# Kernel tuning notes

Measured on AMD Instinct MI355X. Metric: run time of the kernel, lower is better.

The kernel has to match this reference:

```python
import jax, jax.numpy as jnp
import numpy as np

# Dimensions (match init_kwargs / input_specs)
B, T, H, S, R, E = 4, 2048, 1024, 512, 16, 4
F = 6 + 2 * R           # engine_state_feature_dim
ETA = 0.1               # impression_rate
ACC_DECAY = 0.99        # accumulator EMA decay
EPS = 1e-6


def setup_inputs() -> dict:
    key = jax.random.key(0)
    ks = jax.random.split(key, 20)
    n = jax.random.normal
    x = n(ks[0], (B, T, H), jnp.float32)
    # ComplexLinear signal_proj: hidden -> state
    sig_Wr = n(ks[1], (H, S), jnp.float32) / np.sqrt(H).astype(np.float32)
    sig_Wi = n(ks[2], (H, S), jnp.float32) / np.sqrt(H).astype(np.float32)
    sig_br = jnp.zeros((S,), jnp.float32)
    sig_bi = jnp.zeros((S,), jnp.float32)
    # Per-engine complex state projection [E, S, R] and diagonal complex decay [E, R]
    A_r = n(ks[3], (E, S, R), jnp.float32) / np.sqrt(S).astype(np.float32)
    A_i = n(ks[4], (E, S, R), jnp.float32) / np.sqrt(S).astype(np.float32)
    mag = 0.90 + 0.09 * jax.random.uniform(ks[5], (E, R), jnp.float32)
    ph = (2.0 * np.pi) * jax.random.uniform(ks[6], (E, R), jnp.float32)
    lam_r = mag * jnp.cos(ph)
    lam_i = mag * jnp.sin(ph)
    # Per-engine ComplexLinear: feature(F) -> hidden(H)
    eh_Wr = n(ks[7], (E, F, H), jnp.float32) / np.sqrt(F).astype(np.float32)
    eh_Wi = n(ks[8], (E, F, H), jnp.float32) / np.sqrt(F).astype(np.float32)
    eh_br = jnp.zeros((E, H), jnp.float32)
    eh_bi = jnp.zeros((E, H), jnp.float32)
    # Engine fusion ComplexLinear: E*H -> H
    fu_Wr = n(ks[9], (E * H, H), jnp.float32) / np.sqrt(E * H).astype(np.float32)
    fu_Wi = n(ks[10], (E * H, H), jnp.float32) / np.sqrt(E * H).astype(np.float32)
    fu_br = jnp.zeros((H,), jnp.float32)
    fu_bi = jnp.zeros((H,), jnp.float32)
    # Gate: Linear(4H -> H)
    g_W = n(ks[11], (4 * H, H), jnp.float32) / np.sqrt(4 * H).astype(np.float32)
    g_b = jnp.zeros((H,), jnp.float32)
    return dict(x=x, sig_Wr=sig_Wr, sig_Wi=sig_Wi, sig_br=sig_br, sig_bi=sig_bi,
                A_r=A_r, A_i=A_i, lam_r=lam_r, lam_i=lam_i,
                eh_Wr=eh_Wr, eh_Wi=eh_Wi, eh_br=eh_br, eh_bi=eh_bi,
                fu_Wr=fu_Wr, fu_Wi=fu_Wi, fu_br=fu_br, fu_bi=fu_bi,
                g_W=g_W, g_b=g_b)


def _run_engines(ur, ui, lam_r, lam_i):
    """Complex diagonal recurrence over time for all engines jointly.
    ur, ui: [E,B,T,R] complex drive. Returns per-step features [E,B,T,F] (real, imag)."""
    lr = lam_r[:, None, :]  # [E,1,R]
    li = lam_i[:, None, :]

    def step(carry, u):
        hr, hi, acc = carry                      # [E,B,R], [E,B,R], [E,B]
        ur_t, ui_t = u                           # [E,B,R]
        nhr = (1.0 - ETA) * (lr * hr - li * hi) + ETA * ur_t
        nhi = (1.0 - ETA) * (lr * hi + li * hr) + ETA * ui_t
        mag2 = nhr * nhr + nhi * nhi             # [E,B,R]
        m_mean = jnp.mean(mag2, axis=-1)         # [E,B]
        nacc = ACC_DECAY * acc + (1.0 - ACC_DECAY) * m_mean
        inv = jax.lax.rsqrt(m_mean + EPS)[..., None]
        hnr, hni = nhr * inv, nhi * inv          # rms-normalized complex state
        z = jnp.zeros_like(m_mean)
        scal_r = jnp.stack([hnr.mean(-1), hni.mean(-1),
                            jnp.sqrt(m_mean + EPS),
                            jnp.sqrt(jnp.max(mag2, axis=-1) + EPS),
                            nacc, jnp.log1p(nacc)], axis=-1)   # [E,B,6]
        scal_i = jnp.stack([hni.mean(-1), -hnr.mean(-1), z, z, z, z], axis=-1)
        fr = jnp.concatenate([scal_r, hnr, hni], axis=-1)      # [E,B,F]
        fi = jnp.concatenate([scal_i, hni, -hnr], axis=-1)
        return (nhr, nhi, nacc), (fr, fi)

    init = (jnp.zeros((E, B, R), ur.dtype), jnp.zeros((E, B, R), ur.dtype),
            jnp.zeros((E, B), ur.dtype))
    u_seq = (jnp.moveaxis(ur, 2, 0), jnp.moveaxis(ui, 2, 0))   # [T,E,B,R]
    _, (frs, fis) = jax.lax.scan(step, init, u_seq)
    return jnp.moveaxis(frs, 0, 2), jnp.moveaxis(fis, 0, 2)    # [E,B,T,F]


def reference(x, sig_Wr, sig_Wi, sig_br, sig_bi, A_r, A_i, lam_r, lam_i,
              eh_Wr, eh_Wi, eh_br, eh_bi, fu_Wr, fu_Wi, fu_br, fu_bi, g_W, g_b):
    # Complex signal projection of real input: z = (Wr + i Wi)^T x + b
    zr = x @ sig_Wr + sig_br                     # [B,T,S]
    zi = x @ sig_Wi + sig_bi
    # Complex per-engine drive u = A^H-style complex matmul: [E,B,T,R]
    ur = jnp.einsum('bts,esr->ebtr', zr, A_r) - jnp.einsum('bts,esr->ebtr', zi, A_i)
    ui = jnp.einsum('bts,esr->ebtr', zr, A_i) + jnp.einsum('bts,esr->ebtr', zi, A_r)
    fr, fi = _run_engines(ur, ui, lam_r, lam_i)  # [E,B,T,F]
    # Per-engine ComplexLinear feature -> hidden
    yr = (jnp.einsum('ebtf,efh->ebth', fr, eh_Wr)
          - jnp.einsum('ebtf,efh->ebth', fi, eh_Wi)) + eh_br[:, None, None, :]
    yi = (jnp.einsum('ebtf,efh->ebth', fr, eh_Wi)
          + jnp.einsum('ebtf,efh->ebth', fi, eh_Wr)) + eh_bi[:, None, None, :]
    # Concat engines along feature axis -> [B,T,E*H]
    yr_c = jnp.moveaxis(yr, 0, 2).reshape(B, T, E * H)
    yi_c = jnp.moveaxis(yi, 0, 2).reshape(B, T, E * H)
    # Engine fusion ComplexLinear
    frf = yr_c @ fu_Wr - yi_c @ fu_Wi + fu_br    # [B,T,H]
    fif = yr_c @ fu_Wi + yi_c @ fu_Wr + fu_bi
    mag = jnp.sqrt(frf * frf + fif * fif + EPS)
    g = jax.nn.sigmoid(jnp.concatenate([x, frf, fif, mag], axis=-1) @ g_W + g_b)
    return g * frf + (1.0 - g) * x
```

## Files before the change

kernel.cpp:

```cpp
#include <hip/hip_runtime.h>
#include <stdint.h>

#define B_ 4
#define T_ 2048
#define H_ 1024
#define S_ 512
#define R_ 16
#define E_ 4
#define F_ 38
#define BT_ (B_*T_)
#define KF_ 320

typedef __attribute__((ext_vector_type(8))) __bf16 bf16x8;
typedef __attribute__((ext_vector_type(4))) float f32x4;

static __device__ __forceinline__ unsigned short f2bf(float f) {
    unsigned int u = __float_as_uint(f);
    unsigned int r = (u + 0x7fffu + ((u >> 16) & 1u)) >> 16;
    return (unsigned short)r;
}

static __device__ __forceinline__ void gload_lds16(const unsigned short* g, unsigned short* l) {
    __builtin_amdgcn_global_load_lds(
        (const __attribute__((address_space(1))) unsigned int*)g,
        (__attribute__((address_space(3))) unsigned int*)l, 16, 0, 0);
}

template<int EPI, int DEPTH>
__global__ __launch_bounds__(256) void k_gemm(
    const unsigned short* __restrict__ A, int lda,
    const unsigned short* __restrict__ BT, int ldb,
    float* __restrict__ C, int ldc,
    const float* __restrict__ bias, int K,
    size_t sA, size_t sB, size_t sC, size_t sA2, size_t sB2, int nbx,
    const float* __restrict__ aux1, const float* __restrict__ aux2,
    unsigned short* __restrict__ auxO)
{
    const int z1 = blockIdx.z >> 2, z0 = blockIdx.z & 3;
    A  += (size_t)z1 * sA + (size_t)z0 * sA2;
    BT += (size_t)z1 * sB + (size_t)z0 * sB2;
    C  += (size_t)z1 * sC;

    int bx, by;
    {
        const int f = blockIdx.x;
        const int nwg = gridDim.x;
        int s;
        if ((nwg & 7) == 0) {
            const int q = nwg >> 3;
            s = (f & 7) * q + (f >> 3);
        } else s = f;
        by = s / nbx; bx = s - by * nbx;
    }

    __shared__ unsigned short As[DEPTH * 4096];
    __shared__ unsigned short Bs[DEPTH * 4096];
    const int tid = threadIdx.x;
    const int l = tid & 63;
    const int wv = tid >> 6;
    const int wm = wv >> 1, wn = wv & 1;
    const int m16 = l & 15, kg = l >> 4;
    const size_t bm = (size_t)by * 128;
    const size_t bn = (size_t)bx * 128;

    const int slab0 = wv * 2, slab1 = wv * 2 + 1;
    const int rIn = l >> 2;
    const int kOff = (l & 3) * 8;
    const unsigned short* gA0 = A + (bm + slab0 * 16 + rIn) * (size_t)lda + kOff;
    const unsigned short* gA1 = A + (bm + slab1 * 16 + rIn) * (size_t)lda + kOff;
    const unsigned short* gB0 = BT + (bn + slab0 * 16 + rIn) * (size_t)ldb + kOff;
    const unsigned short* gB1 = BT + (bn + slab1 * 16 + rIn) * (size_t)ldb + kOff;
    const int sOffA0 = slab0 * 512, sOffA1 = slab1 * 512;

    f32x4 acc[4][4];
#pragma unroll
    for (int i = 0; i < 4; ++i)
#pragma unroll
        for (int j = 0; j < 4; ++j) acc[i][j] = (f32x4){0.f, 0.f, 0.f, 0.f};

    const int nkt = K >> 5;
#pragma unroll
    for (int p = 0; p < DEPTH - 1; ++p) {
        if (p < nkt) {
            const int o = p * 4096;
            gload_lds16(gA0, As + o + sOffA0);
            gload_lds16(gA1, As + o + sOffA1);
            gload_lds16(gB0, Bs + o + sOffA0);
            gload_lds16(gB1, Bs + o + sOffA1);
            gA0 += 32; gA1 += 32; gB0 += 32; gB1 += 32;
        }
    }

    for (int kt = 0; kt < nkt; ++kt) {
        __builtin_amdgcn_s_barrier();
        if (kt + DEPTH - 1 < nkt) {
            const int o = ((kt + DEPTH - 1) % DEPTH) * 4096;
            gload_lds16(gA0, As + o + sOffA0);
            gload_lds16(gA1, As + o + sOffA1);
            gload_lds16(gB0, Bs + o + sOffA0);
            gload_lds16(gB1, Bs + o + sOffA1);
            gA0 += 32; gA1 += 32; gB0 += 32; gB1 += 32;
        }
        const int rem = nkt - 1 - kt;
        const int ahead = rem < (DEPTH - 1) ? rem : (DEPTH - 1);
        if (ahead >= 3)      asm volatile("s_waitcnt vmcnt(12)" ::: "memory");
        else if (ahead == 2) asm volatile("s_waitcnt vmcnt(8)" ::: "memory");
        else if (ahead == 1) asm volatile("s_waitcnt vmcnt(4)" ::: "memory");
        else                 asm volatile("s_waitcnt vmcnt(0)" ::: "memory");
        __builtin_amdgcn_s_barrier();

        const int cur = (kt % DEPTH) * 4096;
        bf16x8 af[4], bfr[4];
#pragma unroll
        for (int i = 0; i < 4; ++i)
            af[i] = *(const bf16x8*)&As[cur + (wm * 64 + i * 16 + m16) * 32 + kg * 8];
#pragma unroll
        for (int j = 0; j < 4; ++j)
            bfr[j] = *(const bf16x8*)&Bs[cur + (wn * 64 + j * 16 + m16) * 32 + kg * 8];
#pragma unroll
        for (int i = 0; i < 4; ++i)
#pragma unroll
            for (int j = 0; j < 4; ++j)
                acc[i][j] = __builtin_amdgcn_mfma_f32_16x16x32_bf16(af[i], bfr[j], acc[i][j], 0, 0, 0);
    }

#pragma unroll
    for (int j = 0; j < 4; ++j) {
        const size_t col = bn + wn * 64 + j * 16 + m16;
        const float bv = (EPI == 1 || EPI == 4) ? 0.f : (bias ? bias[col] : 0.f);
#pragma unroll
        for (int i = 0; i < 4; ++i) {
            const size_t row0 = bm + wm * 64 + i * 16 + kg * 4;
#pragma unroll
            for (int p = 0; p < 4; ++p) {
                const size_t row = row0 + p;
                if constexpr (EPI == 0) {
                    C[row * (size_t)ldc + col] = acc[i][j][p] + bv;
                } else if constexpr (EPI == 1) {
                    atomicAdd(&C[row * (size_t)ldc + col], acc[i][j][p]);
                } else if constexpr (EPI == 4) {
                    atomicAdd(&C[col * (size_t)ldc + row], acc[i][j][p]);
                } else if constexpr (EPI == 2) {
                    const float v = acc[i][j][p] + bv;
                    const float w = __shfl_xor(v, 1, 64);
                    const int h = (int)(col >> 1);
                    if ((col & 1) == 0) {
                        C[row * 1024 + h] = v;
                        auxO[row * 4096 + 1024 + h] = f2bf(v);
                    } else {
                        auxO[row * 4096 + 2048 + h] = f2bf(v);
                        auxO[row * 4096 + 3072 + h] = f2bf(sqrtf(w * w + v * v + 1e-6f));
                    }
                } else {
                    const float z = acc[i][j][p] + bv;
                    const float g = 1.f / (1.f + __expf(-z));
                    const float fr = aux1[row * 1024 + col];
                    const float xv = aux2[row * 1024 + col];
                    C[row * 1024 + col] = fmaf(g, fr - xv, xv);
                }
            }
        }
    }
}

__global__ __launch_bounds__(256) void k_cast_x(const float* __restrict__ x,
                                                unsigned short* __restrict__ Abig)
{
    const int gid = blockIdx.x * 256 + threadIdx.x;
    const int row = gid >> 8;
    const int c4 = (gid & 255) << 2;
    float4 v = *(const float4*)&x[(size_t)row * H_ + c4];
    ushort4 o;
    o.x = f2bf(v.x); o.y = f2bf(v.y); o.z = f2bf(v.z); o.w = f2bf(v.w);
    *(ushort4*)&Abig[(size_t)row * 4096 + c4] = o;
}

__global__ __launch_bounds__(256) void k_gwt(const float* __restrict__ gW,
                                             unsigned short* __restrict__ gWT)
{
    __shared__ float tile[32][33];
    const int tx = threadIdx.x & 31, ty = threadIdx.x >> 5;
    const int k0 = blockIdx.x * 32, n0 = blockIdx.y * 32;
#pragma unroll
    for (int q = 0; q < 4; ++q) {
        int kk = ty * 4 + q;
        tile[kk][tx] = gW[(size_t)(k0 + kk) * H_ + n0 + tx];
    }
    __syncthreads();
#pragma unroll
    for (int q = 0; q < 4; ++q) {
        int nn = ty * 4 + q;
        gWT[(size_t)(n0 + nn) * 4096 + k0 + tx] = f2bf(tile[tx][nn]);
    }
}

__global__ __launch_bounds__(64) void k_wu(const float* __restrict__ sigWr,
                                           const float* __restrict__ sigWi,
                                           const float* __restrict__ A_r,
                                           const float* __restrict__ A_i,
                                           unsigned short* __restrict__ WuT)
{
    __shared__ float swr[S_], swi[S_];
    const int h = blockIdx.x;
    const int tid = threadIdx.x;
    for (int s = tid; s < S_; s += 64) {
        swr[s] = sigWr[(size_t)h * S_ + s];
        swi[s] = sigWi[(size_t)h * S_ + s];
    }
    __syncthreads();
    const int e = tid >> 4, r = tid & 15;
    float a0 = 0.f, a1 = 0.f;
    for (int s = 0; s < S_; ++s) {
        float ar = A_r[((size_t)(e * S_ + s)) * R_ + r];
        float ai = A_i[((size_t)(e * S_ + s)) * R_ + r];
        float wr = swr[s], wi = swi[s];
        a0 += wr * ar - wi * ai;
        a1 += wr * ai + wi * ar;
    }
    WuT[(size_t)tid * H_ + h] = f2bf(a0);
    WuT[(size_t)(64 + tid) * H_ + h] = f2bf(a1);
}

__global__ __launch_bounds__(64) void k_bu(const float* __restrict__ sigbr,
                                           const float* __restrict__ sigbi,
                                           const float* __restrict__ A_r,
                                           const float* __restrict__ A_i,
                                           float* __restrict__ b_u)
{
    const int n = blockIdx.x;
    const int lane = threadIdx.x;
    const int m = n & 63;
    const int e = m >> 4, r = m & 15;
    const bool hi = n >= 64;
    float acc = 0.f;
    for (int s = lane; s < S_; s += 64) {
        float ar = A_r[((size_t)(e * S_ + s)) * R_ + r];
        float ai = A_i[((size_t)(e * S_ + s)) * R_ + r];
        float br = sigbr[s], bi = sigbi[s];
        acc += hi ? (br * ai + bi * ar) : (br * ar - bi * ai);
    }
#pragma unroll
    for (int st = 32; st; st >>= 1) acc += __shfl_down(acc, st, 64);
    if (lane == 0) b_u[n] = acc;
}

__global__ __launch_bounds__(256) void k_uinit(const float* __restrict__ b_u,
                                               float* __restrict__ U)
{
    const int gid = blockIdx.x * 256 + threadIdx.x;
    U[gid] = b_u[gid >> 13];
}

__global__ __launch_bounds__(256) void k_prepA(const float* __restrict__ ehWr,
                                               const float* __restrict__ ehWi,
                                               const float* __restrict__ ehbr,
                                               const float* __restrict__ ehbi,
                                               unsigned short* __restrict__ Ac)
{
    const int gid = blockIdx.x * 256 + threadIdx.x;
    const int e = gid >> 16;
    const int rem = gid & 65535;
    const int row = rem >> 9;
    const int k = (rem & 511) << 2;
    float4 f = {0.f, 0.f, 0.f, 0.f};
    if (row < F_) {
        const float* src = (k < 1024) ? ehWr + ((size_t)(e * F_ + row)) * 1024 + k
                                      : ehWi + ((size_t)(e * F_ + row)) * 1024 + (k - 1024);
        f = *(const float4*)src;
    } else if (row == F_) {
        const float* src = (k < 1024) ? ehbr + (size_t)e * 1024 + k
                                      : ehbi + (size_t)e * 1024 + (k - 1024);
        f = *(const float4*)src;
    }
    ushort4 o;
    o.x = f2bf(f.x); o.y = f2bf(f.y); o.z = f2bf(f.z); o.w = f2bf(f.w);
    *(ushort4*)&Ac[(size_t)gid * 4] = o;
}

__global__ __launch_bounds__(256) void k_prepB(const float* __restrict__ fuWr,
                                               const float* __restrict__ fuWi,
                                               unsigned short* __restrict__ Bc)
{
    __shared__ float tR[32][33], tI[32][33];
    const int e = blockIdx.z;
    const int k0 = blockIdx.x * 32;
    const int h0 = blockIdx.y * 32;
    const int tx = threadIdx.x & 31, ty = threadIdx.x >> 5;
    const float* fr = fuWr + ((size_t)e * 1024 + k0) * 1024 + h0;
    const float* fi = fuWi + ((size_t)e * 1024 + k0) * 1024 + h0;
#pragma unroll
    for (int q = 0; q < 4; ++q) {
        int kk = ty * 4 + q;
        tR[kk][tx] = fr[(size_t)kk * 1024 + tx];
        tI[kk][tx] = fi[(size_t)kk * 1024 + tx];
    }
    __syncthreads();
    unsigned short* Be = Bc + (size_t)e * 2048 * 2048;
#pragma unroll
    for (int q = 0; q < 4; ++q) {
        int rr = ty * 4 + q;
        float vR = tR[tx][rr], vI = tI[tx][rr];
        size_t rowLo = (size_t)(h0 + rr) * 2048;
        size_t rowHi = (size_t)(1024 + h0 + rr) * 2048;
        Be[rowLo + k0 + tx]        = f2bf(vR);
        Be[rowLo + 1024 + k0 + tx] = f2bf(-vI);
        Be[rowHi + k0 + tx]        = f2bf(vI);
        Be[rowHi + 1024 + k0 + tx] = f2bf(vR);
    }
}

__global__ __launch_bounds__(256) void k_w2t(const float* __restrict__ C,
                                             unsigned short* __restrict__ W2T)
{
    const int gid = blockIdx.x * 256 + threadIdx.x;
    const int n = gid / KF_;
    const int k = gid - n * KF_;
    const int h = n >> 1;
    const int s = n & 1;
    float v = 0.f;
    if (k < 304) {
        const int fp = (k < 152) ? k : k - 152;
        const int e = fp / F_;
        const int f = fp - e * F_;
        const float* Ce = C + ((size_t)e * 128 + f) * 2048;
        const float mr = Ce[h], mi = Ce[1024 + h];
        if (s == 0) v = (k < 152) ? mr : -mi;
        else        v = (k < 152) ? mi :  mr;
    }
    W2T[gid] = f2bf(v);
}

__global__ __launch_bounds__(256) void k_b2(const float* __restrict__ fubr,
                                            const float* __restrict__ fubi,
                                            const float* __restrict__ C,
                                            float* __restrict__ b2)
{
    const int n = blockIdx.x * 256 + threadIdx.x;
    const int h = n >> 1;
    const int s = n & 1;
    const int colOld = s * 1024 + h;
    float v = s ? fubi[h] : fubr[h];
#pragma unroll
    for (int e = 0; e < 4; ++e)
        v += C[(size_t)e * 128 * 2048 + (size_t)F_ * 2048 + colOld];
    b2[n] = v;
}

__global__ __launch_bounds__(64) void k_scan(const float* __restrict__ U,
                                             const float* __restrict__ lam_r,
                                             const float* __restrict__ lam_i,
                                             float* __restrict__ Hr, float* __restrict__ Hi)
{
    const int wid = blockIdx.x;
    const int b = wid >> 6, ch = wid & 63;
    const int lane = threadIdx.x;
    const float cr = 0.9f * lam_r[ch];
    const float ci = 0.9f * lam_i[ch];
    const float* Ur = U + (size_t)ch * BT_ + (size_t)b * T_;
    const float* Uc = U + (size_t)(64 + ch) * BT_ + (size_t)b * T_;
    const int t0 = lane * 32;
    float ur[32], ui[32];
#pragma unroll
    for (int q = 0; q < 8; ++q) {
        float4 vr = *(const float4*)&Ur[t0 + q * 4];
        float4 vi = *(const float4*)&Uc[t0 + q * 4];
        ur[q*4+0]=vr.x; ur[q*4+1]=vr.y; ur[q*4+2]=vr.z; ur[q*4+3]=vr.w;
        ui[q*4+0]=vi.x; ui[q*4+1]=vi.y; ui[q*4+2]=vi.z; ui[q*4+3]=vi.w;
    }
    float hr = 0.f, hi = 0.f;
#pragma unroll
    for (int j = 0; j < 32; ++j) {
        float nr = fmaf(cr, hr, fmaf(-ci, hi, 0.1f * ur[j]));
        float ni = fmaf(cr, hi, fmaf(ci, hr, 0.1f * ui[j]));
        hr = nr; hi = ni;
    }
    float dr = cr, di = ci;
#pragma unroll
    for (int q = 0; q < 5; ++q) { float t = dr*dr - di*di; di = 2.f*dr*di; dr = t; }
    float xr = hr, xi = hi;
#pragma unroll
    for (int st = 1; st < 64; st <<= 1) {
        float yr = __shfl_up(xr, (unsigned)st, 64);
        float yi = __shfl_up(xi, (unsigned)st, 64);
        if (lane >= st) {
            float nxr = fmaf(dr, yr, fmaf(-di, yi, xr));
            float nxi = fmaf(dr, yi, fmaf(di, yr, xi));
            xr = nxr; xi = nxi;
        }
        float t = dr*dr - di*di; di = 2.f*dr*di; dr = t;
    }
    float ir = __shfl_up(xr, 1u, 64);
    float ii = __shfl_up(xi, 1u, 64);
    if (lane == 0) { ir = 0.f; ii = 0.f; }
    hr = ir; hi = ii;
    float* HrB = Hr + (size_t)b * T_ * 64;
    float* HiB = Hi + (size_t)b * T_ * 64;
#pragma unroll
    for (int j = 0; j < 32; ++j) {
        float nr = fmaf(cr, hr, fmaf(-ci, hi, 0.1f * ur[j]));
        float ni = fmaf(cr, hi, fmaf(ci, hr, 0.1f * ui[j]));
        HrB[(size_t)(t0 + j) * 64 + ch] = nr;
        HiB[(size_t)(t0 + j) * 64 + ch] = ni;
        hr = nr; hi = ni;
    }
}

__global__ __launch_bounds__(256) void k_feat(const float* __restrict__ Hr,
                                              const float* __restrict__ Hi,
                                              unsigned short* __restrict__ Fcat,
                                              float* __restrict__ Mbuf)
{
    const int gid = blockIdx.x * 256 + threadIdx.x;
    const int e = gid & 3;
    const int bt = gid >> 2;
    const float* hr = Hr + (size_t)bt * 64 + e * 16;
    const float* hi = Hi + (size_t)bt * 64 + e * 16;
    float nr[16], ni[16];
#pragma unroll
    for (int q = 0; q < 4; ++q) {
        float4 vr = ((const float4*)hr)[q];
        float4 vi = ((const float4*)hi)[q];
        nr[q*4+0]=vr.x; nr[q*4+1]=vr.y; nr[q*4+2]=vr.z; nr[q*4+3]=vr.w;
        ni[q*4+0]=vi.x; ni[q*4+1]=vi.y; ni[q*4+2]=vi.z; ni[q*4+3]=vi.w;
    }
    float sum = 0.f, mx = 0.f, sr = 0.f, si = 0.f;
#pragma unroll
    for (int i = 0; i < 16; ++i) {
        float m2 = nr[i] * nr[i] + ni[i] * ni[i];
        sum += m2; mx = fmaxf(mx, m2);
        sr += nr[i]; si += ni[i];
    }
    const float mm = sum * 0.0625f;
    const float inv = rsqrtf(mm + 1e-6f);
    const int b = bt >> 11, t = bt & (T_ - 1);
    Mbuf[(size_t)(e * 4 + b) * T_ + t] = mm;
    unsigned short* Fp = Fcat + (size_t)bt * KF_;
    const int br = e * F_, bi2 = 152 + e * F_;
    const float mhr = sr * 0.0625f * inv;
    const float mhi = si * 0.0625f * inv;
    Fp[br + 0] = f2bf(mhr);
    Fp[br + 1] = f2bf(mhi);
    Fp[br + 2] = f2bf(sqrtf(mm + 1e-6f));
    Fp[br + 3] = f2bf(sqrtf(mx + 1e-6f));
    Fp[bi2 + 0] = f2bf(mhi);
    Fp[bi2 + 1] = f2bf(-mhr);
#pragma unroll
    for (int i = 0; i < 16; ++i) {
        float a = nr[i] * inv, c = ni[i] * inv;
        Fp[br + 6 + i]   = f2bf(a);
        Fp[br + 22 + i]  = f2bf(c);
        Fp[bi2 + 6 + i]  = f2bf(c);
        Fp[bi2 + 22 + i] = f2bf(-a);
    }
}

__global__ __launch_bounds__(256) void k_acc(const float* __restrict__ Mbuf,
                                             unsigned short* __restrict__ Fcat)
{
    const int w = blockIdx.x * 4 + (threadIdx.x >> 6);
    const int lane = threadIdx.x & 63;
    const int e = w >> 2, b = w & 3;
    const float* mp = Mbuf + (size_t)(e * 4 + b) * T_ + lane * 32;
    float m[32];
#pragma unroll
    for (int j = 0; j < 32; ++j) m[j] = mp[j];
    float s = 0.f;
#pragma unroll
    for (int j = 0; j < 32; ++j) s = fmaf(0.99f, s, 0.01f * m[j]);
    float d = 0.99f;
#pragma unroll
    for (int q = 0; q < 5; ++q) d = d * d;
    float x = s;
#pragma unroll
    for (int st = 1; st < 64; st <<= 1) {
        float y = __shfl_up(x, (unsigned)st, 64);
        if (lane >= st) x = fmaf(d, y, x);
        d = d * d;
    }
    float init = __shfl_up(x, 1u, 64);
    if (lane == 0) init = 0.f;
    float acc = init;
#pragma unroll
    for (int j = 0; j < 32; ++j) {
        acc = fmaf(0.99f, acc, 0.01f * m[j]);
        const int t = lane * 32 + j;
        size_t ro = ((size_t)(b * T_ + t)) * KF_ + e * F_;
        Fcat[ro + 4] = f2bf(acc);
        Fcat[ro + 5] = f2bf(log1pf(acc));
    }
}

extern "C" void kernel_launch(void* const* d_in, const int* in_sizes, int n_in,
                              void* d_out, int out_size, void* d_ws, size_t ws_size,
                              hipStream_t stream)
{
    const float* x     = (const float*)d_in[0];
    const float* sigWr = (const float*)d_in[1];
    const float* sigWi = (const float*)d_in[2];
    const float* sigbr = (const float*)d_in[3];
    const float* sigbi = (const float*)d_in[4];
    const float* A_r   = (const float*)d_in[5];
    const float* A_i   = (const float*)d_in[6];
    const float* lam_r = (const float*)d_in[7];
    const float* lam_i = (const float*)d_in[8];
    const float* ehWr  = (const float*)d_in[9];
    const float* ehWi  = (const float*)d_in[10];
    const float* ehbr  = (const float*)d_in[11];
    const float* ehbi  = (const float*)d_in[12];
    const float* fuWr  = (const float*)d_in[13];
    const float* fuWi  = (const float*)d_in[14];
    const float* fubr  = (const float*)d_in[15];
    const float* fubi  = (const float*)d_in[16];
    const float* gW    = (const float*)d_in[17];
    const float* gb    = (const float*)d_in[18];

    char* ws = (char*)d_ws;
    size_t off = 0;
    auto alloc = [&](size_t bytes) -> void* {
        void* p = ws + off;
        off = (off + bytes + 255) & ~(size_t)255;
        return p;
    };
    unsigned short* Abig = (unsigned short*)alloc((size_t)BT_ * 4096 * 2);
    float* FRFr          = (float*)alloc((size_t)BT_ * 1024 * 4);
    unsigned short* Fcat = (unsigned short*)alloc((size_t)BT_ * KF_ * 2);
    float* U             = (float*)alloc((size_t)BT_ * 128 * 4);
    float* Hr            = (float*)alloc((size_t)BT_ * 64 * 4);
    float* Hi            = (float*)alloc((size_t)BT_ * 64 * 4);
    float* Mbuf          = (float*)alloc((size_t)16 * T_ * 4);
    unsigned short* WuT  = (unsigned short*)alloc((size_t)128 * H_ * 2);
    float* b_u           = (float*)alloc(128 * 4);
    unsigned short* W2T  = (unsigned short*)alloc((size_t)2048 * KF_ * 2);
    float* b2            = (float*)alloc(2048 * 4);
    unsigned short* gWT  = (unsigned short*)alloc((size_t)H_ * 4096 * 2);
    unsigned short* Acomp= (unsigned short*)alloc((size_t)4 * 128 * 2048 * 2);
    unsigned short* Bcomp= (unsigned short*)alloc((size_t)4 * 2048 * 2048 * 2);
    float* Ccomp         = (float*)alloc((size_t)4 * 128 * 2048 * 4);
    if (off > ws_size) return;

    hipMemsetAsync(Fcat, 0, (size_t)BT_ * KF_ * 2, stream);
    hipMemsetAsync(Ccomp, 0, (size_t)4 * 128 * 2048 * 4, stream);

    k_cast_x<<<dim3(BT_ * H_ / 4 / 256), dim3(256), 0, stream>>>(x, Abig);
    k_gwt<<<dim3(128, 32), dim3(256), 0, stream>>>(gW, gWT);
    k_wu<<<dim3(H_), dim3(64), 0, stream>>>(sigWr, sigWi, A_r, A_i, WuT);
    k_bu<<<dim3(128), dim3(64), 0, stream>>>(sigbr, sigbi, A_r, A_i, b_u);
    k_prepA<<<dim3(1024), dim3(256), 0, stream>>>(ehWr, ehWi, ehbr, ehbi, Acomp);
    k_prepB<<<dim3(32, 32, 4), dim3(256), 0, stream>>>(fuWr, fuWi, Bcomp);

    k_gemm<1, 4><<<dim3(16, 1, 16), dim3(256), 0, stream>>>(
        Acomp, 2048, Bcomp, 2048, Ccomp, 2048, (const float*)nullptr, 512,
        (size_t)128 * 2048, (size_t)2048 * 2048, (size_t)128 * 2048,
        (size_t)512, (size_t)512, 16, nullptr, nullptr, nullptr);

    k_w2t<<<dim3(2048 * KF_ / 256), dim3(256), 0, stream>>>(Ccomp, W2T);
    k_b2<<<dim3(8), dim3(256), 0, stream>>>(fubr, fubi, Ccomp, b2);

    k_uinit<<<dim3(BT_ * 128 / 256), dim3(256), 0, stream>>>(b_u, U);
    k_gemm<4, 4><<<dim3(64, 1, 4), dim3(256), 0, stream>>>(
        Abig, 4096, WuT, H_, U, BT_, (const float*)nullptr, 256,
        (size_t)0, (size_t)0, (size_t)0, (size_t)256, (size_t)256, 1,
        nullptr, nullptr, nullptr);

    k_scan<<<dim3(B_ * 64), dim3(64), 0, stream>>>(U, lam_r, lam_i, Hr, Hi);
    k_feat<<<dim3(BT_ * E_ / 256), dim3(256), 0, stream>>>(Hr, Hi, Fcat, Mbuf);
    k_acc<<<dim3(4), dim3(256), 0, stream>>>(Mbuf, Fcat);

    k_gemm<2, 2><<<dim3(1024, 1, 1), dim3(256), 0, stream>>>(
        Fcat, KF_, W2T, KF_, FRFr, 1024, b2, KF_,
        (size_t)0, (size_t)0, (size_t)0, (size_t)0, (size_t)0, 16,
        nullptr, nullptr, Abig);

    k_gemm<3, 4><<<dim3(512, 1, 1), dim3(256), 0, stream>>>(
        Abig, 4096, gWT, 4096, (float*)d_out, 1024, gb, 4096,
        (size_t)0, (size_t)0, (size_t)0, (size_t)0, (size_t)0, 8,
        FRFr, x, nullptr);
}
```

Measured before the change: 418.1 us.

## Replace direct global-to-LDS multistage pipeline with register-staged double buffering

The GEMM kernel drops the `global_load_lds` path and its DEPTH-stage LDS ring. It now loads tiles into registers two k-steps ahead, writes them into a two-slot LDS double buffer while the current slot is read, and unrolls the k-loop by two. The intent is a more predictable load/compute overlap with less LDS and a single barrier per step. The cost is extra VGPRs for staging and explicit LDS write instructions. The unroll by two assumes an even k-tile count, which holds for all current launches.

```diff
diff --git a/kernel.cpp b/kernel.cpp
--- a/kernel.cpp
+++ b/kernel.cpp
@@ -20,13 +20,7 @@
     return (unsigned short)r;
 }
 
-static __device__ __forceinline__ void gload_lds16(const unsigned short* g, unsigned short* l) {
-    __builtin_amdgcn_global_load_lds(
-        (const __attribute__((address_space(1))) unsigned int*)g,
-        (__attribute__((address_space(3))) unsigned int*)l, 16, 0, 0);
-}
-
-template<int EPI, int DEPTH>
+template<int EPI>
 __global__ __launch_bounds__(256) void k_gemm(
     const unsigned short* __restrict__ A, int lda,
     const unsigned short* __restrict__ BT, int ldb,
@@ -53,8 +47,8 @@
         by = s / nbx; bx = s - by * nbx;
     }
 
-    __shared__ unsigned short As[DEPTH * 4096];
-    __shared__ unsigned short Bs[DEPTH * 4096];
+    __shared__ unsigned short As[2 * 4096];
+    __shared__ unsigned short Bs[2 * 4096];
     const int tid = threadIdx.x;
     const int l = tid & 63;
     const int wv = tid >> 6;
@@ -63,14 +57,14 @@
     const size_t bm = (size_t)by * 128;
     const size_t bn = (size_t)bx * 128;
 
-    const int slab0 = wv * 2, slab1 = wv * 2 + 1;
-    const int rIn = l >> 2;
-    const int kOff = (l & 3) * 8;
-    const unsigned short* gA0 = A + (bm + slab0 * 16 + rIn) * (size_t)lda + kOff;
-    const unsigned short* gA1 = A + (bm + slab1 * 16 + rIn) * (size_t)lda + kOff;
-    const unsigned short* gB0 = BT + (bn + slab0 * 16 + rIn) * (size_t)ldb + kOff;
-    const unsigned short* gB1 = BT + (bn + slab1 * 16 + rIn) * (size_t)ldb + kOff;
-    const int sOffA0 = slab0 * 512, sOffA1 = slab1 * 512;
+    const int rS = tid >> 2;
+    const int kS = (tid & 3) * 8;
+    const unsigned short* gA0 = A + (bm + rS) * (size_t)lda + kS;
+    const unsigned short* gA1 = gA0 + (size_t)64 * lda;
+    const unsigned short* gB0 = BT + (bn + rS) * (size_t)ldb + kS;
+    const unsigned short* gB1 = gB0 + (size_t)64 * ldb;
+    const int s0 = tid * 8;
+    const int s1 = (256 + tid) * 8;
 
     f32x4 acc[4][4];
 #pragma unroll
@@ -79,50 +73,55 @@
         for (int j = 0; j < 4; ++j) acc[i][j] = (f32x4){0.f, 0.f, 0.f, 0.f};
 
     const int nkt = K >> 5;
-#pragma unroll
-    for (int p = 0; p < DEPTH - 1; ++p) {
-        if (p < nkt) {
-            const int o = p * 4096;
-            gload_lds16(gA0, As + o + sOffA0);
-            gload_lds16(gA1, As + o + sOffA1);
-            gload_lds16(gB0, Bs + o + sOffA0);
-            gload_lds16(gB1, Bs + o + sOffA1);
-            gA0 += 32; gA1 += 32; gB0 += 32; gB1 += 32;
-        }
-    }
-
-    for (int kt = 0; kt < nkt; ++kt) {
-        __builtin_amdgcn_s_barrier();
-        if (kt + DEPTH - 1 < nkt) {
-            const int o = ((kt + DEPTH - 1) % DEPTH) * 4096;
-            gload_lds16(gA0, As + o + sOffA0);
-            gload_lds16(gA1, As + o + sOffA1);
-            gload_lds16(gB0, Bs + o + sOffA0);
-            gload_lds16(gB1, Bs + o + sOffA1);
-            gA0 += 32; gA1 += 32; gB0 += 32; gB1 += 32;
-        }
-        const int rem = nkt - 1 - kt;
-        const int ahead = rem < (DEPTH - 1) ? rem : (DEPTH - 1);
-        if (ahead >= 3)      asm volatile("s_waitcnt vmcnt(12)" ::: "memory");
-        else if (ahead == 2) asm volatile("s_waitcnt vmcnt(8)" ::: "memory");
-        else if (ahead == 1) asm volatile("s_waitcnt vmcnt(4)" ::: "memory");
-        else                 asm volatile("s_waitcnt vmcnt(0)" ::: "memory");
-        __builtin_amdgcn_s_barrier();
-
-        const int cur = (kt % DEPTH) * 4096;
-        bf16x8 af[4], bfr[4];
-#pragma unroll
-        for (int i = 0; i < 4; ++i)
-            af[i] = *(const bf16x8*)&As[cur + (wm * 64 + i * 16 + m16) * 32 + kg * 8];
-#pragma unroll
-        for (int j = 0; j < 4; ++j)
-            bfr[j] = *(const bf16x8*)&Bs[cur + (wn * 64 + j * 16 + m16) * 32 + kg * 8];
-#pragma unroll
-        for (int i = 0; i < 4; ++i)
-#pragma unroll
-            for (int j = 0; j < 4; ++j)
-                acc[i][j] = __builtin_amdgcn_mfma_f32_16x16x32_bf16(af[i], bfr[j], acc[i][j], 0, 0, 0);
-    }
+
+    uint4 xA0, xA1, xB0, xB1;
+    uint4 yA0, yA1, yB0, yB1;
+
+#define GLOAD(A0,A1,B0,B1) do { \
+        A0 = *(const uint4*)gA0; A1 = *(const uint4*)gA1; \
+        B0 = *(const uint4*)gB0; B1 = *(const uint4*)gB1; \
+        gA0 += 32; gA1 += 32; gB0 += 32; gB1 += 32; } while (0)
+
+#define FENCE_BAR() do { \
+        asm volatile("s_waitcnt lgkmcnt(0)" ::: "memory"); \
+        __builtin_amdgcn_sched_barrier(0); \
+        __builtin_amdgcn_s_barrier(); \
+        __builtin_amdgcn_sched_barrier(0); } while (0)
+
+#define GSTEP(KT, CB, LA0,LA1,LB0,LB1, WA0,WA1,WB0,WB1) do { \
+        if ((KT) + 2 < nkt) { GLOAD(LA0,LA1,LB0,LB1); } \
+        bf16x8 af[4], bfr[4]; \
+        _Pragma("unroll") \
+        for (int i = 0; i < 4; ++i) \
+            af[i] = *(const bf16x8*)&As[(CB) + (wm * 64 + i * 16 + m16) * 32 + kg * 8]; \
+        _Pragma("unroll") \
+        for (int j = 0; j < 4; ++j) \
+            bfr[j] = *(const bf16x8*)&Bs[(CB) + (wn * 64 + j * 16 + m16) * 32 + kg * 8]; \
+        if ((KT) + 1 < nkt) { \
+            const int nb = 4096 - (CB); \
+            *(uint4*)&As[nb + s0] = WA0; *(uint4*)&As[nb + s1] = WA1; \
+            *(uint4*)&Bs[nb + s0] = WB0; *(uint4*)&Bs[nb + s1] = WB1; \
+        } \
+        _Pragma("unroll") \
+        for (int i = 0; i < 4; ++i) \
+            _Pragma("unroll") \
+            for (int j = 0; j < 4; ++j) \
+                acc[i][j] = __builtin_amdgcn_mfma_f32_16x16x32_bf16(af[i], bfr[j], acc[i][j], 0, 0, 0); \
+        FENCE_BAR(); } while (0)
+
+    GLOAD(xA0, xA1, xB0, xB1);
+    GLOAD(yA0, yA1, yB0, yB1);
+    *(uint4*)&As[s0] = xA0; *(uint4*)&As[s1] = xA1;
+    *(uint4*)&Bs[s0] = xB0; *(uint4*)&Bs[s1] = xB1;
+    FENCE_BAR();
+
+    for (int kt = 0; kt < nkt; kt += 2) {
+        GSTEP(kt,     0,    xA0,xA1,xB0,xB1,  yA0,yA1,yB0,yB1);
+        GSTEP(kt + 1, 4096, yA0,yA1,yB0,yB1,  xA0,xA1,xB0,xB1);
+    }
+#undef GSTEP
+#undef GLOAD
+#undef FENCE_BAR
 
 #pragma unroll
     for (int j = 0; j < 4; ++j) {
@@ -548,7 +547,7 @@
     k_prepA<<<dim3(1024), dim3(256), 0, stream>>>(ehWr, ehWi, ehbr, ehbi, Acomp);
     k_prepB<<<dim3(32, 32, 4), dim3(256), 0, stream>>>(fuWr, fuWi, Bcomp);
 
-    k_gemm<1, 4><<<dim3(16, 1, 16), dim3(256), 0, stream>>>(
+    k_gemm<1><<<dim3(16, 1, 16), dim3(256), 0, stream>>>(
         Acomp, 2048, Bcomp, 2048, Ccomp, 2048, (const float*)nullptr, 512,
         (size_t)128 * 2048, (size_t)2048 * 2048, (size_t)128 * 2048,
         (size_t)512, (size_t)512, 16, nullptr, nullptr, nullptr);
@@ -557,7 +556,7 @@
     k_b2<<<dim3(8), dim3(256), 0, stream>>>(fubr, fubi, Ccomp, b2);
 
     k_uinit<<<dim3(BT_ * 128 / 256), dim3(256), 0, stream>>>(b_u, U);
-    k_gemm<4, 4><<<dim3(64, 1, 4), dim3(256), 0, stream>>>(
+    k_gemm<4><<<dim3(64, 1, 4), dim3(256), 0, stream>>>(
         Abig, 4096, WuT, H_, U, BT_, (const float*)nullptr, 256,
         (size_t)0, (size_t)0, (size_t)0, (size_t)256, (size_t)256, 1,
         nullptr, nullptr, nullptr);
@@ -566,12 +565,12 @@
     k_feat<<<dim3(BT_ * E_ / 256), dim3(256), 0, stream>>>(Hr, Hi, Fcat, Mbuf);
     k_acc<<<dim3(4), dim3(256), 0, stream>>>(Mbuf, Fcat);
 
-    k_gemm<2, 2><<<dim3(1024, 1, 1), dim3(256), 0, stream>>>(
+    k_gemm<2><<<dim3(1024, 1, 1), dim3(256), 0, stream>>>(
         Fcat, KF_, W2T, KF_, FRFr, 1024, b2, KF_,
         (size_t)0, (size_t)0, (size_t)0, (size_t)0, (size_t)0, 16,
         nullptr, nullptr, Abig);
 
-    k_gemm<3, 4><<<dim3(512, 1, 1), dim3(256), 0, stream>>>(
+    k_gemm<3><<<dim3(512, 1, 1), dim3(256), 0, stream>>>(
         Abig, 4096, gWT, 4096, (float*)d_out, 1024, gb, 4096,
         (size_t)0, (size_t)0, (size_t)0, (size_t)0, (size_t)0, 8,
         FRFr, x, nullptr);
```

New measurement: 420.1 us. About the same (+0.5%).

## Replace multi-stage async LDS pipeline with register-prefetch single-buffer GEMM loop

Applied to the files above, without the earlier changes.

The GEMM main loop no longer uses the DEPTH-stage global_load_lds asynchronous pipeline with manual vmcnt waits. Each K tile is now loaded into registers one iteration ahead, written to a single LDS buffer between two __syncthreads, and then consumed by the MFMA loop. This cuts LDS usage, which may allow more blocks per CU and simplifies the synchronisation. The cost is less latency hiding from a shallower pipeline, extra VGPRs for the staged data, and two barriers per K step.

```diff
diff --git a/kernel.cpp b/kernel.cpp
--- a/kernel.cpp
+++ b/kernel.cpp
@@ -20,13 +20,7 @@
     return (unsigned short)r;
 }
 
-static __device__ __forceinline__ void gload_lds16(const unsigned short* g, unsigned short* l) {
-    __builtin_amdgcn_global_load_lds(
-        (const __attribute__((address_space(1))) unsigned int*)g,
-        (__attribute__((address_space(3))) unsigned int*)l, 16, 0, 0);
-}
-
-template<int EPI, int DEPTH>
+template<int EPI>
 __global__ __launch_bounds__(256) void k_gemm(
     const unsigned short* __restrict__ A, int lda,
     const unsigned short* __restrict__ BT, int ldb,
@@ -53,8 +47,8 @@
         by = s / nbx; bx = s - by * nbx;
     }
 
-    __shared__ unsigned short As[DEPTH * 4096];
-    __shared__ unsigned short Bs[DEPTH * 4096];
+    __shared__ unsigned short As[128 * 32];
+    __shared__ unsigned short Bs[128 * 32];
     const int tid = threadIdx.x;
     const int l = tid & 63;
     const int wv = tid >> 6;
@@ -63,14 +57,12 @@
     const size_t bm = (size_t)by * 128;
     const size_t bn = (size_t)bx * 128;
 
-    const int slab0 = wv * 2, slab1 = wv * 2 + 1;
-    const int rIn = l >> 2;
-    const int kOff = (l & 3) * 8;
-    const unsigned short* gA0 = A + (bm + slab0 * 16 + rIn) * (size_t)lda + kOff;
-    const unsigned short* gA1 = A + (bm + slab1 * 16 + rIn) * (size_t)lda + kOff;
-    const unsigned short* gB0 = BT + (bn + slab0 * 16 + rIn) * (size_t)ldb + kOff;
-    const unsigned short* gB1 = BT + (bn + slab1 * 16 + rIn) * (size_t)ldb + kOff;
-    const int sOffA0 = slab0 * 512, sOffA1 = slab1 * 512;
+    const int rS = tid >> 2;
+    const int kS = (tid & 3) * 8;
+    const unsigned short* pA0 = A + (bm + rS) * (size_t)lda + kS;
+    const unsigned short* pA1 = pA0 + (size_t)64 * lda;
+    const unsigned short* pB0 = BT + (bn + rS) * (size_t)ldb + kS;
+    const unsigned short* pB1 = pB0 + (size_t)64 * ldb;
 
     f32x4 acc[4][4];
 #pragma unroll
@@ -78,45 +70,35 @@
 #pragma unroll
         for (int j = 0; j < 4; ++j) acc[i][j] = (f32x4){0.f, 0.f, 0.f, 0.f};
 
+    uint4 ra0 = *(const uint4*)pA0;
+    uint4 ra1 = *(const uint4*)pA1;
+    uint4 rb0 = *(const uint4*)pB0;
+    uint4 rb1 = *(const uint4*)pB1;
+
+    const int s0 = tid * 8;
+    const int s1 = (256 + tid) * 8;
     const int nkt = K >> 5;
-#pragma unroll
-    for (int p = 0; p < DEPTH - 1; ++p) {
-        if (p < nkt) {
-            const int o = p * 4096;
-            gload_lds16(gA0, As + o + sOffA0);
-            gload_lds16(gA1, As + o + sOffA1);
-            gload_lds16(gB0, Bs + o + sOffA0);
-            gload_lds16(gB1, Bs + o + sOffA1);
-            gA0 += 32; gA1 += 32; gB0 += 32; gB1 += 32;
+    for (int kt = 0; kt < nkt; ++kt) {
+        __syncthreads();
+        *(uint4*)&As[s0] = ra0;
+        *(uint4*)&As[s1] = ra1;
+        *(uint4*)&Bs[s0] = rb0;
+        *(uint4*)&Bs[s1] = rb1;
+        if (kt + 1 < nkt) {
+            pA0 += 32; pA1 += 32; pB0 += 32; pB1 += 32;
+            ra0 = *(const uint4*)pA0;
+            ra1 = *(const uint4*)pA1;
+            rb0 = *(const uint4*)pB0;
+            rb1 = *(const uint4*)pB1;
         }
-    }
-
-    for (int kt = 0; kt < nkt; ++kt) {
-        __builtin_amdgcn_s_barrier();
-        if (kt + DEPTH - 1 < nkt) {
-            const int o = ((kt + DEPTH - 1) % DEPTH) * 4096;
-            gload_lds16(gA0, As + o + sOffA0);
-            gload_lds16(gA1, As + o + sOffA1);
-            gload_lds16(gB0, Bs + o + sOffA0);
-            gload_lds16(gB1, Bs + o + sOffA1);
-            gA0 += 32; gA1 += 32; gB0 += 32; gB1 += 32;
-        }
-        const int rem = nkt - 1 - kt;
-        const int ahead = rem < (DEPTH - 1) ? rem : (DEPTH - 1);
-        if (ahead >= 3)      asm volatile("s_waitcnt vmcnt(12)" ::: "memory");
-        else if (ahead == 2) asm volatile("s_waitcnt vmcnt(8)" ::: "memory");
-        else if (ahead == 1) asm volatile("s_waitcnt vmcnt(4)" ::: "memory");
-        else                 asm volatile("s_waitcnt vmcnt(0)" ::: "memory");
-        __builtin_amdgcn_s_barrier();
-
-        const int cur = (kt % DEPTH) * 4096;
+        __syncthreads();
         bf16x8 af[4], bfr[4];
 #pragma unroll
         for (int i = 0; i < 4; ++i)
-            af[i] = *(const bf16x8*)&As[cur + (wm * 64 + i * 16 + m16) * 32 + kg * 8];
+            af[i] = *(const bf16x8*)&As[(wm * 64 + i * 16 + m16) * 32 + kg * 8];
 #pragma unroll
         for (int j = 0; j < 4; ++j)
-            bfr[j] = *(const bf16x8*)&Bs[cur + (wn * 64 + j * 16 + m16) * 32 + kg * 8];
+            bfr[j] = *(const bf16x8*)&Bs[(wn * 64 + j * 16 + m16) * 32 + kg * 8];
 #pragma unroll
         for (int i = 0; i < 4; ++i)
 #pragma unroll
@@ -548,7 +530,7 @@
     k_prepA<<<dim3(1024), dim3(256), 0, stream>>>(ehWr, ehWi, ehbr, ehbi, Acomp);
     k_prepB<<<dim3(32, 32, 4), dim3(256), 0, stream>>>(fuWr, fuWi, Bcomp);
 
-    k_gemm<1, 4><<<dim3(16, 1, 16), dim3(256), 0, stream>>>(
+    k_gemm<1><<<dim3(16, 1, 16), dim3(256), 0, stream>>>(
         Acomp, 2048, Bcomp, 2048, Ccomp, 2048, (const float*)nullptr, 512,
         (size_t)128 * 2048, (size_t)2048 * 2048, (size_t)128 * 2048,
         (size_t)512, (size_t)512, 16, nullptr, nullptr, nullptr);
@@ -557,7 +539,7 @@
     k_b2<<<dim3(8), dim3(256), 0, stream>>>(fubr, fubi, Ccomp, b2);
 
     k_uinit<<<dim3(BT_ * 128 / 256), dim3(256), 0, stream>>>(b_u, U);
-    k_gemm<4, 4><<<dim3(64, 1, 4), dim3(256), 0, stream>>>(
+    k_gemm<4><<<dim3(64, 1, 4), dim3(256), 0, stream>>>(
         Abig, 4096, WuT, H_, U, BT_, (const float*)nullptr, 256,
         (size_t)0, (size_t)0, (size_t)0, (size_t)256, (size_t)256, 1,
         nullptr, nullptr, nullptr);
@@ -566,12 +548,12 @@
     k_feat<<<dim3(BT_ * E_ / 256), dim3(256), 0, stream>>>(Hr, Hi, Fcat, Mbuf);
     k_acc<<<dim3(4), dim3(256), 0, stream>>>(Mbuf, Fcat);
 
-    k_gemm<2, 2><<<dim3(1024, 1, 1), dim3(256), 0, stream>>>(
+    k_gemm<2><<<dim3(1024, 1, 1), dim3(256), 0, stream>>>(
         Fcat, KF_, W2T, KF_, FRFr, 1024, b2, KF_,
         (size_t)0, (size_t)0, (size_t)0, (size_t)0, (size_t)0, 16,
         nullptr, nullptr, Abig);
 
-    k_gemm<3, 4><<<dim3(512, 1, 1), dim3(256), 0, stream>>>(
+    k_gemm<3><<<dim3(512, 1, 1), dim3(256), 0, stream>>>(
         Abig, 4096, gWT, 4096, (float*)d_out, 1024, gb, 4096,
         (size_t)0, (size_t)0, (size_t)0, (size_t)0, (size_t)0, 8,
         FRFr, x, nullptr);
```

Result: faster. 398.4 us (-4.7%).
